# Performance work log

Hardware: AMD Instinct MI355X
Metric: run time of the kernel (lower is better)

The kernel has to match this reference:

```python
import jax, jax.numpy as jnp
import numpy as np

B, L, D = 4, 4096, 2048
E = 64           # num_experts
K = 2            # top_k
AUX_W = 0.01     # aux_loss_weight


def setup_inputs() -> dict:
    key = jax.random.key(0)
    kx, kw = jax.random.split(key)
    x = jax.random.normal(kx, (B, L, D), dtype=jnp.float32)
    W = jax.random.normal(kw, (E, D), dtype=jnp.float32) * 0.02  # nn.init.normal_(std=0.02)
    return {"x": x, "W": W}


def reference(x, W):
    # gate: logits [B, L, E]
    logits = jnp.einsum('bld,ed->ble', x, W)
    # full softmax over experts (used for aux loss)
    probs = jax.nn.softmax(logits, axis=-1)
    # top-k selection and renormalized weights
    top_k_logits, top_k_indices = jax.lax.top_k(logits, K)      # [B, L, K]
    top_k_weights = jax.nn.softmax(top_k_logits, axis=-1)       # [B, L, K]
    # load-balance aux loss (Switch-style): uses top-1 expert assignment
    expert_mask = jax.nn.one_hot(top_k_indices[..., 0], E, dtype=jnp.float32)  # [B, L, E]
    expert_fraction = expert_mask.mean(axis=(0, 1))              # [E]
    prob_fraction = probs.mean(axis=(0, 1))                      # [E]
    aux_loss = E * jnp.sum(expert_fraction * prob_fraction) * AUX_W
    return top_k_indices, top_k_weights, aux_loss
```

## Files before the change

### kernel.cpp

```cpp
#include <hip/hip_runtime.h>

#define D_DIM 2048
#define E_NUM 64
#define M_TOK 16384
#define BM 64
#define BK 64
#define SPLITK 2
#define KSPLIT (D_DIM / SPLITK)
#define XS_STRIDE 68


__global__ __launch_bounds__(128) void init_kernel(float* __restrict__ g) {
    g[threadIdx.x] = 0.0f;
}

__global__ __launch_bounds__(256, 2) void gemm_kernel(
    const float* __restrict__ x, const float* __restrict__ W,
    float* __restrict__ part)
{
    __shared__ float xs[BM * XS_STRIDE];
    __shared__ float wl[BK * E_NUM];

    const int tid  = threadIdx.x;
    const int tx   = tid & 15;
    const int ty   = tid >> 4;
    const int lrow = tid >> 4;
    const int lk4  = (tid & 15) << 2;
    const long tokbase = (long)blockIdx.x * BM;
    const int  kbase   = blockIdx.y * KSPLIT;

    double accd[4][4];
    float  accc[4][4];
    #pragma unroll
    for (int i = 0; i < 4; ++i)
        #pragma unroll
        for (int j = 0; j < 4; ++j) { accd[i][j] = 0.0; accc[i][j] = 0.0f; }

    for (int it = 0; it < KSPLIT / BK; ++it) {
        const int k0 = kbase + it * BK;
        #pragma unroll
        for (int p = 0; p < 4; ++p) {
            const int row = p * 16 + lrow;
            const float4 xv = *(const float4*)&x[(tokbase + row) * D_DIM + k0 + lk4];
            *(float4*)&xs[row * XS_STRIDE + lk4] = xv;
        }
        #pragma unroll
        for (int p = 0; p < 4; ++p) {
            const int e  = p * 16 + lrow;
            const float4 wv = *(const float4*)&W[(long)e * D_DIM + k0 + lk4];
            const int cb = e >> 2, ci = e & 3;
            wl[(lk4 + 0) * E_NUM + ((cb ^ ((lk4 + 0) & 15)) << 2) + ci] = wv.x;
            wl[(lk4 + 1) * E_NUM + ((cb ^ ((lk4 + 1) & 15)) << 2) + ci] = wv.y;
            wl[(lk4 + 2) * E_NUM + ((cb ^ ((lk4 + 2) & 15)) << 2) + ci] = wv.z;
            wl[(lk4 + 3) * E_NUM + ((cb ^ ((lk4 + 3) & 15)) << 2) + ci] = wv.w;
        }
        __syncthreads();
        #pragma unroll
        for (int kf = 0; kf < 4; ++kf) {
            #pragma unroll
            for (int kb = 0; kb < 4; ++kb) {
                const int kkb = kf * 16 + kb * 4;
                float xrf[16];
                #pragma unroll
                for (int i = 0; i < 4; ++i) {
                    const float4 v = *(const float4*)&xs[(ty * 4 + i) * XS_STRIDE + kkb];
                    xrf[i * 4 + 0] = v.x; xrf[i * 4 + 1] = v.y;
                    xrf[i * 4 + 2] = v.z; xrf[i * 4 + 3] = v.w;
                }
                #pragma unroll
                for (int k2 = 0; k2 < 4; ++k2) {
                    const int kk = kkb + k2;
                    const float4 wq = *(const float4*)&wl[kk * E_NUM + ((tx ^ (kk & 15)) << 2)];
                    const float wqf[4] = { wq.x, wq.y, wq.z, wq.w };
                    #pragma unroll
                    for (int i = 0; i < 4; ++i)
                        #pragma unroll
                        for (int j = 0; j < 4; ++j)
                            accc[i][j] += xrf[i * 4 + k2] * wqf[j];
                }
            }
            #pragma unroll
            for (int i = 0; i < 4; ++i)
                #pragma unroll
                for (int j = 0; j < 4; ++j) { accd[i][j] += (double)accc[i][j]; accc[i][j] = 0.0f; }
        }
        __syncthreads();
    }
    float* dst = part + (size_t)blockIdx.y * ((size_t)M_TOK * E_NUM);
    #pragma unroll
    for (int i = 0; i < 4; ++i) {
        const long m = tokbase + ty * 4 + i;
        float4 v;
        v.x = (float)accd[i][0]; v.y = (float)accd[i][1];
        v.z = (float)accd[i][2]; v.w = (float)accd[i][3];
        *(float4*)&dst[m * E_NUM + (tx << 2)] = v;
    }
}

__global__ __launch_bounds__(256) void topk_kernel(
    const float* __restrict__ part, float* __restrict__ out,
    float* __restrict__ gprob, float* __restrict__ gcnt)
{
    __shared__ float pacc[4][E_NUM];
    __shared__ float cacc[4][E_NUM];
    const int w    = threadIdx.x >> 6;
    const int lane = threadIdx.x & 63;
    pacc[w][lane] = 0.0f;
    cacc[w][lane] = 0.0f;
    const int gw = blockIdx.x * 4 + w;

    for (int i = 0; i < 16; ++i) {
        const int t = gw * 16 + i;
        const float l = part[(size_t)t * E_NUM + lane]
                      + part[((size_t)M_TOK + t) * E_NUM + lane];
        float m1 = l; int i1 = lane;
        #pragma unroll
        for (int off = 32; off > 0; off >>= 1) {
            const float ov = __shfl_xor(m1, off, 64);
            const int   oi = __shfl_xor(i1, off, 64);
            if (ov > m1 || (ov == m1 && oi < i1)) { m1 = ov; i1 = oi; }
        }
        const float p = __expf(l - m1);
        float s = p;
        #pragma unroll
        for (int off = 32; off > 0; off >>= 1) s += __shfl_xor(s, off, 64);
        pacc[w][lane] += p / s;
        if (lane == i1) cacc[w][lane] += 1.0f;
        const float lm = (lane == i1) ? -1e30f : l;
        float m2 = lm; int i2 = lane;
        #pragma unroll
        for (int off = 32; off > 0; off >>= 1) {
            const float ov = __shfl_xor(m2, off, 64);
            const int   oi = __shfl_xor(i2, off, 64);
            if (ov > m2 || (ov == m2 && oi < i2)) { m2 = ov; i2 = oi; }
        }
        if (lane == 0) {
            out[2 * t]     = (float)i1;
            out[2 * t + 1] = (float)i2;
            const float w1 = 1.0f / (1.0f + __expf(m2 - m1));
            out[2 * M_TOK + 2 * t]     = w1;
            out[2 * M_TOK + 2 * t + 1] = 1.0f - w1;
        }
    }
    __syncthreads();
    if (threadIdx.x < E_NUM) {
        const int e = threadIdx.x;
        atomicAdd(&gprob[e], pacc[0][e] + pacc[1][e] + pacc[2][e] + pacc[3][e]);
        atomicAdd(&gcnt[e],  cacc[0][e] + cacc[1][e] + cacc[2][e] + cacc[3][e]);
    }
}

__global__ __launch_bounds__(64) void aux_kernel(
    const float* __restrict__ gprob, const float* __restrict__ gcnt,
    float* __restrict__ out)
{
    const int lane = threadIdx.x;
    float v = gprob[lane] * gcnt[lane];
    #pragma unroll
    for (int off = 32; off > 0; off >>= 1) v += __shfl_xor(v, off, 64);
    if (lane == 0)
        out[4 * M_TOK] = 64.0f * 0.01f * v / ((float)M_TOK * (float)M_TOK);
}

extern "C" void kernel_launch(void* const* d_in, const int* in_sizes, int n_in,
                              void* d_out, int out_size, void* d_ws, size_t ws_size,
                              hipStream_t stream)
{
    const float* x = (const float*)d_in[0];
    const float* W = (const float*)d_in[1];
    float* out   = (float*)d_out;
    float* part  = (float*)d_ws;
    float* gprob = part + (size_t)SPLITK * M_TOK * E_NUM;
    float* gcnt  = gprob + E_NUM;

    init_kernel<<<1, 128, 0, stream>>>(gprob);
    gemm_kernel<<<dim3(M_TOK / BM, SPLITK), 256, 0, stream>>>(x, W, part);
    topk_kernel<<<M_TOK / 64, 256, 0, stream>>>(part, out, gprob, gcnt);
    aux_kernel<<<1, 64, 0, stream>>>(gprob, gcnt, out);
}
```

Before: 273.6 us.

## Drop LDS staging in gating GEMM, raise split-K, per-token top-k without atomics

The GEMM no longer stages x and W through shared memory. Each thread loads float4 slices of its own 4 token rows and 4 expert rows straight from global memory, with no barriers and a higher occupancy bound, and split-K rises to 4 when the workspace allows. The top-k kernel moves from one wavefront per token to one thread per token, doing a serial top-2 and softmax over 64 registers. Aux statistics are now reduced per block into workspace and summed by the aux kernel, replacing the global atomics and the init kernel. The risk is that direct global loads lose the shared-memory reuse, since each x and W element is re-fetched by 16 threads, and the per-thread top-k uses many registers.

```diff
diff --git a/kernel.cpp b/kernel.cpp
--- a/kernel.cpp
+++ b/kernel.cpp
@@ -4,88 +4,63 @@
 #define E_NUM 64
 #define M_TOK 16384
 #define BM 64
-#define BK 64
-#define SPLITK 2
-#define KSPLIT (D_DIM / SPLITK)
-#define XS_STRIDE 68
 
 
-__global__ __launch_bounds__(128) void init_kernel(float* __restrict__ g) {
-    g[threadIdx.x] = 0.0f;
-}
+__global__ __launch_bounds__(256, 4) void gemm_kernel(
+    const float* __restrict__ x, const float* __restrict__ W,
+    float* __restrict__ part, int ksplit)
+{
+    const int tid = threadIdx.x;
+    const int tx  = tid & 15;
+    const int ty  = tid >> 4;
+    const long tokbase = (long)blockIdx.x * BM;
+    const int  kbase   = blockIdx.y * ksplit;
 
-__global__ __launch_bounds__(256, 2) void gemm_kernel(
-    const float* __restrict__ x, const float* __restrict__ W,
-    float* __restrict__ part)
-{
-    __shared__ float xs[BM * XS_STRIDE];
-    __shared__ float wl[BK * E_NUM];
-
-    const int tid  = threadIdx.x;
-    const int tx   = tid & 15;
-    const int ty   = tid >> 4;
-    const int lrow = tid >> 4;
-    const int lk4  = (tid & 15) << 2;
-    const long tokbase = (long)blockIdx.x * BM;
-    const int  kbase   = blockIdx.y * KSPLIT;
+    const float* xp[4];
+    const float* wp[4];
+    #pragma unroll
+    for (int i = 0; i < 4; ++i) {
+        xp[i] = x + (tokbase + (long)(ty * 4 + i)) * D_DIM + kbase;
+        wp[i] = W + (long)(tx * 4 + i) * D_DIM + kbase;
+    }
 
     double accd[4][4];
-    float  accc[4][4];
     #pragma unroll
     for (int i = 0; i < 4; ++i)
         #pragma unroll
-        for (int j = 0; j < 4; ++j) { accd[i][j] = 0.0; accc[i][j] = 0.0f; }
+        for (int j = 0; j < 4; ++j) accd[i][j] = 0.0;
 
-    for (int it = 0; it < KSPLIT / BK; ++it) {
-        const int k0 = kbase + it * BK;
+    for (int kc = 0; kc < ksplit; kc += 32) {
+        float accc[4][4];
         #pragma unroll
-        for (int p = 0; p < 4; ++p) {
-            const int row = p * 16 + lrow;
-            const float4 xv = *(const float4*)&x[(tokbase + row) * D_DIM + k0 + lk4];
-            *(float4*)&xs[row * XS_STRIDE + lk4] = xv;
-        }
+        for (int i = 0; i < 4; ++i)
+            #pragma unroll
+            for (int j = 0; j < 4; ++j) accc[i][j] = 0.0f;
+
         #pragma unroll
-        for (int p = 0; p < 4; ++p) {
-            const int e  = p * 16 + lrow;
-            const float4 wv = *(const float4*)&W[(long)e * D_DIM + k0 + lk4];
-            const int cb = e >> 2, ci = e & 3;
-            wl[(lk4 + 0) * E_NUM + ((cb ^ ((lk4 + 0) & 15)) << 2) + ci] = wv.x;
-            wl[(lk4 + 1) * E_NUM + ((cb ^ ((lk4 + 1) & 15)) << 2) + ci] = wv.y;
-            wl[(lk4 + 2) * E_NUM + ((cb ^ ((lk4 + 2) & 15)) << 2) + ci] = wv.z;
-            wl[(lk4 + 3) * E_NUM + ((cb ^ ((lk4 + 3) & 15)) << 2) + ci] = wv.w;
-        }
-        __syncthreads();
-        #pragma unroll
-        for (int kf = 0; kf < 4; ++kf) {
+        for (int kb = 0; kb < 8; ++kb) {
+            const int ko = kc + kb * 4;
+            float4 xv[4], wv[4];
             #pragma unroll
-            for (int kb = 0; kb < 4; ++kb) {
-                const int kkb = kf * 16 + kb * 4;
-                float xrf[16];
-                #pragma unroll
-                for (int i = 0; i < 4; ++i) {
-                    const float4 v = *(const float4*)&xs[(ty * 4 + i) * XS_STRIDE + kkb];
-                    xrf[i * 4 + 0] = v.x; xrf[i * 4 + 1] = v.y;
-                    xrf[i * 4 + 2] = v.z; xrf[i * 4 + 3] = v.w;
-                }
-                #pragma unroll
-                for (int k2 = 0; k2 < 4; ++k2) {
-                    const int kk = kkb + k2;
-                    const float4 wq = *(const float4*)&wl[kk * E_NUM + ((tx ^ (kk & 15)) << 2)];
-                    const float wqf[4] = { wq.x, wq.y, wq.z, wq.w };
-                    #pragma unroll
-                    for (int i = 0; i < 4; ++i)
-                        #pragma unroll
-                        for (int j = 0; j < 4; ++j)
-                            accc[i][j] += xrf[i * 4 + k2] * wqf[j];
-                }
-            }
+            for (int i = 0; i < 4; ++i) xv[i] = *(const float4*)(xp[i] + ko);
+            #pragma unroll
+            for (int j = 0; j < 4; ++j) wv[j] = *(const float4*)(wp[j] + ko);
             #pragma unroll
             for (int i = 0; i < 4; ++i)
                 #pragma unroll
-                for (int j = 0; j < 4; ++j) { accd[i][j] += (double)accc[i][j]; accc[i][j] = 0.0f; }
+                for (int j = 0; j < 4; ++j) {
+                    accc[i][j] += xv[i].x * wv[j].x;
+                    accc[i][j] += xv[i].y * wv[j].y;
+                    accc[i][j] += xv[i].z * wv[j].z;
+                    accc[i][j] += xv[i].w * wv[j].w;
+                }
         }
-        __syncthreads();
+        #pragma unroll
+        for (int i = 0; i < 4; ++i)
+            #pragma unroll
+            for (int j = 0; j < 4; ++j) accd[i][j] += (double)accc[i][j];
     }
+
     float* dst = part + (size_t)blockIdx.y * ((size_t)M_TOK * E_NUM);
     #pragma unroll
     for (int i = 0; i < 4; ++i) {
@@ -97,68 +72,82 @@
     }
 }
 
-__global__ __launch_bounds__(256) void topk_kernel(
+__global__ __launch_bounds__(64) void topk_kernel(
     const float* __restrict__ part, float* __restrict__ out,
-    float* __restrict__ gprob, float* __restrict__ gcnt)
+    float* __restrict__ blockp, float* __restrict__ blockc, int nsplit)
 {
-    __shared__ float pacc[4][E_NUM];
-    __shared__ float cacc[4][E_NUM];
-    const int w    = threadIdx.x >> 6;
-    const int lane = threadIdx.x & 63;
-    pacc[w][lane] = 0.0f;
-    cacc[w][lane] = 0.0f;
-    const int gw = blockIdx.x * 4 + w;
+    __shared__ float red[64 * 68];
+    __shared__ int   i1s[64];
+    const int  lane = threadIdx.x;
+    const long t    = (long)blockIdx.x * 64 + lane;
 
-    for (int i = 0; i < 16; ++i) {
-        const int t = gw * 16 + i;
-        const float l = part[(size_t)t * E_NUM + lane]
-                      + part[((size_t)M_TOK + t) * E_NUM + lane];
-        float m1 = l; int i1 = lane;
+    float l[64];
+    #pragma unroll
+    for (int j = 0; j < 16; ++j) {
+        const float4 v = *(const float4*)&part[t * E_NUM + j * 4];
+        l[j * 4 + 0] = v.x; l[j * 4 + 1] = v.y; l[j * 4 + 2] = v.z; l[j * 4 + 3] = v.w;
+    }
+    for (int s = 1; s < nsplit; ++s) {
         #pragma unroll
-        for (int off = 32; off > 0; off >>= 1) {
-            const float ov = __shfl_xor(m1, off, 64);
-            const int   oi = __shfl_xor(i1, off, 64);
-            if (ov > m1 || (ov == m1 && oi < i1)) { m1 = ov; i1 = oi; }
-        }
-        const float p = __expf(l - m1);
-        float s = p;
-        #pragma unroll
-        for (int off = 32; off > 0; off >>= 1) s += __shfl_xor(s, off, 64);
-        pacc[w][lane] += p / s;
-        if (lane == i1) cacc[w][lane] += 1.0f;
-        const float lm = (lane == i1) ? -1e30f : l;
-        float m2 = lm; int i2 = lane;
-        #pragma unroll
-        for (int off = 32; off > 0; off >>= 1) {
-            const float ov = __shfl_xor(m2, off, 64);
-            const int   oi = __shfl_xor(i2, off, 64);
-            if (ov > m2 || (ov == m2 && oi < i2)) { m2 = ov; i2 = oi; }
-        }
-        if (lane == 0) {
-            out[2 * t]     = (float)i1;
-            out[2 * t + 1] = (float)i2;
-            const float w1 = 1.0f / (1.0f + __expf(m2 - m1));
-            out[2 * M_TOK + 2 * t]     = w1;
-            out[2 * M_TOK + 2 * t + 1] = 1.0f - w1;
+        for (int j = 0; j < 16; ++j) {
+            const float4 v = *(const float4*)&part[((size_t)s * M_TOK + t) * E_NUM + j * 4];
+            l[j * 4 + 0] += v.x; l[j * 4 + 1] += v.y; l[j * 4 + 2] += v.z; l[j * 4 + 3] += v.w;
         }
     }
+
+    float m1 = -1e30f, m2 = -1e30f; int i1 = 0, i2 = 0;
+    #pragma unroll
+    for (int e = 0; e < 64; ++e) {
+        const float v = l[e];
+        if (v > m1)      { m2 = m1; i2 = i1; m1 = v; i1 = e; }
+        else if (v > m2) { m2 = v;  i2 = e; }
+    }
+
+    float ssum = 0.0f;
+    #pragma unroll
+    for (int e = 0; e < 64; ++e) { l[e] = __expf(l[e] - m1); ssum += l[e]; }
+    const float inv = 1.0f / ssum;
+
+    #pragma unroll
+    for (int j = 0; j < 16; ++j) {
+        float4 v;
+        v.x = l[j * 4 + 0] * inv; v.y = l[j * 4 + 1] * inv;
+        v.z = l[j * 4 + 2] * inv; v.w = l[j * 4 + 3] * inv;
+        *(float4*)&red[lane * 68 + j * 4] = v;
+    }
+    i1s[lane] = i1;
+
+    float2 oi; oi.x = (float)i1; oi.y = (float)i2;
+    *(float2*)&out[2 * t] = oi;
+    const float w1 = 1.0f / (1.0f + __expf(m2 - m1));
+    float2 ow; ow.x = w1; ow.y = 1.0f - w1;
+    *(float2*)&out[2 * M_TOK + 2 * t] = ow;
+
     __syncthreads();
-    if (threadIdx.x < E_NUM) {
-        const int e = threadIdx.x;
-        atomicAdd(&gprob[e], pacc[0][e] + pacc[1][e] + pacc[2][e] + pacc[3][e]);
-        atomicAdd(&gcnt[e],  cacc[0][e] + cacc[1][e] + cacc[2][e] + cacc[3][e]);
-    }
+    float P = 0.0f;
+    #pragma unroll
+    for (int lx = 0; lx < 64; ++lx) P += red[lx * 68 + lane];
+    float C = 0.0f;
+    #pragma unroll
+    for (int lx = 0; lx < 64; ++lx) C += (i1s[lx] == lane) ? 1.0f : 0.0f;
+    blockp[blockIdx.x * E_NUM + lane] = P;
+    blockc[blockIdx.x * E_NUM + lane] = C;
 }
 
 __global__ __launch_bounds__(64) void aux_kernel(
-    const float* __restrict__ gprob, const float* __restrict__ gcnt,
+    const float* __restrict__ blockp, const float* __restrict__ blockc,
     float* __restrict__ out)
 {
-    const int lane = threadIdx.x;
-    float v = gprob[lane] * gcnt[lane];
+    const int e = threadIdx.x;
+    float P = 0.0f, C = 0.0f;
+    for (int b = 0; b < 256; ++b) {
+        P += blockp[b * E_NUM + e];
+        C += blockc[b * E_NUM + e];
+    }
+    float v = P * C;
     #pragma unroll
     for (int off = 32; off > 0; off >>= 1) v += __shfl_xor(v, off, 64);
-    if (lane == 0)
+    if (e == 0)
         out[4 * M_TOK] = 64.0f * 0.01f * v / ((float)M_TOK * (float)M_TOK);
 }
 
@@ -168,13 +157,18 @@
 {
     const float* x = (const float*)d_in[0];
     const float* W = (const float*)d_in[1];
-    float* out   = (float*)d_out;
-    float* part  = (float*)d_ws;
-    float* gprob = part + (size_t)SPLITK * M_TOK * E_NUM;
-    float* gcnt  = gprob + E_NUM;
+    float* out = (float*)d_out;
 
-    init_kernel<<<1, 128, 0, stream>>>(gprob);
-    gemm_kernel<<<dim3(M_TOK / BM, SPLITK), 256, 0, stream>>>(x, W, part);
-    topk_kernel<<<M_TOK / 64, 256, 0, stream>>>(part, out, gprob, gcnt);
-    aux_kernel<<<1, 64, 0, stream>>>(gprob, gcnt, out);
+    const size_t need4 = (size_t)4 * M_TOK * E_NUM * sizeof(float)
+                       + (size_t)2 * 256 * E_NUM * sizeof(float);
+    const int nsplit = (ws_size >= need4) ? 4 : 2;
+    const int ksplit = D_DIM / nsplit;
+
+    float* part   = (float*)d_ws;
+    float* blockp = part + (size_t)nsplit * M_TOK * E_NUM;
+    float* blockc = blockp + 256 * E_NUM;
+
+    gemm_kernel<<<dim3(M_TOK / BM, nsplit), 256, 0, stream>>>(x, W, part, ksplit);
+    topk_kernel<<<256, 64, 0, stream>>>(part, out, blockp, blockc, nsplit);
+    aux_kernel<<<1, 64, 0, stream>>>(blockp, blockc, out);
 }
```

Measured after the change: 557.5 us. +103.8%, slower.
